# Kernel optimization log

Measured on AMD Instinct MI355X. Metric: run time of the kernel, lower is better.

The kernel has to match this reference:

```python
import jax, jax.numpy as jnp
import numpy as np

N = 10000   # nodes
E = 320000  # edges
B = 4       # batch
D = 128     # in_dim == out_dim
H = 4       # heads
DH = D // H # 32, per-head dim
OUT_L = D // H  # per-layer out_fc output dim (out_dim/num_heads)
NEG_SLOPE = 0.1


def setup_inputs() -> dict:
    key = jax.random.key(0)
    ks = jax.random.split(key, 20)
    inp = {
        "features": jax.random.normal(ks[0], (B, N, D), dtype=jnp.float32),
        "src": jax.random.randint(ks[1], (E,), 0, N),
        "dst": jax.random.randint(ks[2], (E,), 0, N),
        "edge_w": jax.random.uniform(ks[3], (E,), dtype=jnp.float32),
    }
    s = 0.05
    for l in range(2):
        k = 4 + 5 * l
        inp[f"fc_w{l}"] = jax.random.normal(ks[k], (D, D), dtype=jnp.float32) * s
        inp[f"al{l}"] = jax.random.normal(ks[k + 1], (H, DH), dtype=jnp.float32) * s
        inp[f"ar{l}"] = jax.random.normal(ks[k + 2], (H, DH), dtype=jnp.float32) * s
        inp[f"out_w{l}"] = jax.random.normal(ks[k + 3], (OUT_L, DH), dtype=jnp.float32) * s
        inp[f"out_b{l}"] = jnp.zeros((OUT_L,), dtype=jnp.float32)
    inp["mlp_w"] = jax.random.normal(ks[14], (D, 2 * D), dtype=jnp.float32) * s
    inp["mlp_b"] = jnp.zeros((D,), dtype=jnp.float32)
    return inp


def _gat_layer(x, src, dst, w, fc_w, al, ar, out_w, out_b):
    # x: [B,N,D]
    feat = jnp.einsum("bnd,ed->bne", x, fc_w).reshape(B, N, H, DH)  # fc, no bias
    el = jnp.einsum("bnhd,hd->bnh", feat, al)  # [B,N,H]
    er = jnp.einsum("bnhd,hd->bnh", feat, ar)
    # per-edge scores, edge-major: [E,B,H]
    e = jnp.moveaxis(el[:, src] + er[:, dst], 1, 0)
    e = jnp.where(e > 0, e, NEG_SLOPE * e)        # LeakyReLU(0.1)
    e = e * w[:, None, None]                      # edge weight applied pre-softmax
    # edge-softmax over incoming edges of each dst node
    m = jax.ops.segment_max(e, dst, num_segments=N)
    m = jnp.where(jnp.isfinite(m), m, 0.0)
    ex = jnp.exp(e - m[dst])
    den = jax.ops.segment_sum(ex, dst, num_segments=N)[dst]
    a = ex / jnp.where(den == 0, 1.0, den)        # [E,B,H]
    # u_mul_e + sum aggregation
    feat_n = jnp.moveaxis(feat, 0, 1)             # [N,B,H,DH]
    msg = feat_n[src] * a[..., None]              # [E,B,H,DH]
    agg = jax.ops.segment_sum(msg, dst, num_segments=N)  # [N,B,H,DH]
    out = jax.nn.relu(jnp.einsum("nbhd,od->nbho", agg, out_w) + out_b)
    # transpose(0,1) then concat heads along feature dim -> [B,N,H*OUT_L]
    return jnp.moveaxis(out, 0, 1).reshape(B, N, H * OUT_L)


def reference(features, src, dst, edge_w,
              fc_w0, al0, ar0, out_w0, out_b0,
              fc_w1, al1, ar1, out_w1, out_b1,
              mlp_w, mlp_b):
    x1 = _gat_layer(features, src, dst, edge_w, fc_w0, al0, ar0, out_w0, out_b0)
    x2 = _gat_layer(x1, src, dst, edge_w, fc_w1, al1, ar1, out_w1, out_b1)
    h = jnp.concatenate([x1, x2], axis=-1)        # [B,N,2*D]
    return jnp.einsum("bnk,ok->bno", h, mlp_w) + mlp_b  # eval mode: dropout off
```

## Files before the change

### kernel.cpp

```cpp
#include <hip/hip_runtime.h>
#include <hip/hip_fp16.h>
#include <float.h>

#define NN 10000
#define EE 320000
#define BB 4
#define DD 128
#define HH 4
#define DHH 32
#define CHUNK 128

union H4 { uint2 u2; __half2 h2[2]; };

typedef _Float16 f16x8 __attribute__((ext_vector_type(8)));
typedef float f32x4 __attribute__((ext_vector_type(4)));

__global__ void pack_weights(const float* __restrict__ fc0, const float* __restrict__ fc1,
                             const float* __restrict__ mlp,
                             __half* __restrict__ bp0, __half* __restrict__ bp1,
                             __half* __restrict__ bpm) {
    int s = blockIdx.x * 256 + threadIdx.x;
    int i = s & 7, l = (s >> 3) & 63, ct = (s >> 9) & 7, kt = s >> 12;
    int k = kt * 32 + 8 * (l >> 4) + i;
    int o = ct * 16 + (l & 15);
    bpm[s] = __float2half(mlp[o * 256 + k]);
    if (s < 16384) {
        bp0[s] = __float2half(fc0[o * 128 + k]);
        bp1[s] = __float2half(fc1[o * 128 + k]);
    }
}

__global__ void count_edges(const int* __restrict__ dst, int* __restrict__ cnt) {
    int e = blockIdx.x * 256 + threadIdx.x;
    if (e < EE) atomicAdd(&cnt[dst[e]], 1);
}

__global__ void scan_kernel(const int* __restrict__ cnt, int* __restrict__ row_off) {
    __shared__ int part[1024];
    int t = threadIdx.x;
    const int CH = 10;
    int loc[CH];
    int s = 0;
#pragma unroll
    for (int j = 0; j < CH; ++j) {
        int i = t * CH + j;
        int v = (i < NN) ? cnt[i] : 0;
        loc[j] = s;
        s += v;
    }
    part[t] = s;
    __syncthreads();
    for (int off = 1; off < 1024; off <<= 1) {
        int v = (t >= off) ? part[t - off] : 0;
        __syncthreads();
        part[t] += v;
        __syncthreads();
    }
    int pre = (t > 0) ? part[t - 1] : 0;
#pragma unroll
    for (int j = 0; j < CH; ++j) {
        int i = t * CH + j;
        if (i < NN) row_off[i] = pre + loc[j];
    }
    if (t == 0) row_off[NN] = part[1023];
}

__global__ void scatter_edges(const int* __restrict__ dst, const int* __restrict__ row_off,
                              int* __restrict__ cursor, int* __restrict__ edge_ids) {
    int e = blockIdx.x * 256 + threadIdx.x;
    if (e < EE) {
        int d = dst[e];
        int p = atomicAdd(&cursor[d], 1);
        edge_ids[row_off[d] + p] = e;
    }
}

template <int K, bool A_HALF, bool HALF_OUT, bool BIAS>
__global__ __launch_bounds__(256) void mfma_gemm(
    const void* __restrict__ A_, int lda,
    const __half* __restrict__ Bp,
    const float* __restrict__ bias,
    __half* __restrict__ outh, float* __restrict__ outf, int ldo) {
    __shared__ __half A_s[64 * K];
    int tid = threadIdx.x;
    int row0 = blockIdx.x * 64;

    if (A_HALF) {
        const __half* A = (const __half*)A_;
#pragma unroll
        for (int it = 0; it < (64 * K / 8) / 256; ++it) {
            int s = it * 256 + tid;
            int r = s / (K / 8), c8 = s % (K / 8);
            uint4 v = *reinterpret_cast<const uint4*>(A + (size_t)(row0 + r) * lda + c8 * 8);
            int byte = (r * K + c8 * 8) * 2;
            byte ^= (r & 7) << 4;
            *reinterpret_cast<uint4*>((char*)A_s + byte) = v;
        }
    } else {
        const float* A = (const float*)A_;
#pragma unroll
        for (int it = 0; it < (64 * K / 4) / 256; ++it) {
            int s = it * 256 + tid;
            int r = s / (K / 4), c4 = s % (K / 4);
            float4 v = *reinterpret_cast<const float4*>(A + (size_t)(row0 + r) * lda + c4 * 4);
            __half h[4];
            h[0] = __float2half(v.x); h[1] = __float2half(v.y);
            h[2] = __float2half(v.z); h[3] = __float2half(v.w);
            int byte = (r * K + c4 * 4) * 2;
            byte ^= (r & 7) << 4;
            *reinterpret_cast<uint2*>((char*)A_s + byte) = *reinterpret_cast<uint2*>(h);
        }
    }
    __syncthreads();

    int l = tid & 63, w = tid >> 6;
    int g = l >> 4, r15 = l & 15;
    f32x4 acc[8] = {};

#pragma unroll
    for (int kt = 0; kt < K / 32; ++kt) {
        int row = w * 16 + r15;
        int byte = (row * K + kt * 32 + 8 * g) * 2;
        byte ^= (row & 7) << 4;
        f16x8 a = *reinterpret_cast<const f16x8*>((const char*)A_s + byte);
        const f16x8* bp = reinterpret_cast<const f16x8*>(Bp) + (size_t)(kt * 8) * 64 + l;
#pragma unroll
        for (int ct = 0; ct < 8; ++ct) {
            f16x8 b = bp[(size_t)ct * 64];
            acc[ct] = __builtin_amdgcn_mfma_f32_16x16x32_f16(a, b, acc[ct], 0, 0, 0);
        }
    }

#pragma unroll
    for (int ct = 0; ct < 8; ++ct) {
        int col = ct * 16 + r15;
#pragma unroll
        for (int reg = 0; reg < 4; ++reg) {
            int row = row0 + w * 16 + g * 4 + reg;
            float v = acc[ct][reg];
            if (BIAS) v += bias[col];
            if (HALF_OUT) outh[(size_t)row * ldo + col] = __float2half(v);
            else outf[(size_t)row * ldo + col] = v;
        }
    }
}

__global__ __launch_bounds__(256) void elr_kernel(
    const __half* __restrict__ feat_h, const float* __restrict__ al,
    const float* __restrict__ ar, float* __restrict__ el, float* __restrict__ er) {
    __shared__ float s_al[128], s_ar[128];
    int tid = threadIdx.x;
    if (tid < 128) s_al[tid] = al[tid];
    else s_ar[tid - 128] = ar[tid - 128];
    __syncthreads();
    int idx = blockIdx.x * 256 + tid;
    if (idx < BB * NN * HH) {
        int h = idx & 3;
        const __half* row = feat_h + (size_t)(idx >> 2) * 128 + h * 32;
        float al_acc = 0.f, ar_acc = 0.f;
#pragma unroll
        for (int q = 0; q < 8; ++q) {
            H4 u;
            u.u2 = *reinterpret_cast<const uint2*>(row + q * 4);
            float2 f0 = __half22float2(u.h2[0]);
            float2 f1 = __half22float2(u.h2[1]);
            int d = h * 32 + q * 4;
            al_acc += f0.x * s_al[d] + f0.y * s_al[d + 1] + f1.x * s_al[d + 2] + f1.y * s_al[d + 3];
            ar_acc += f0.x * s_ar[d] + f0.y * s_ar[d + 1] + f1.x * s_ar[d + 2] + f1.y * s_ar[d + 3];
        }
        el[idx] = al_acc;
        er[idx] = ar_acc;
    }
}

__global__ __launch_bounds__(128) void gat_aggregate(
    const int* __restrict__ row_off, const int* __restrict__ edge_ids,
    const int* __restrict__ src, const float* __restrict__ ew,
    const float* __restrict__ el, const float* __restrict__ er,
    const __half* __restrict__ feat_h, const float* __restrict__ out_w,
    const float* __restrict__ out_b, __half* __restrict__ hcat, int layer_off) {
    __shared__ int s_src[CHUNK];
    __shared__ float s_w[CHUNK];
    __shared__ float s_red[8][16];
    __shared__ float s_m[16];
    __shared__ float s_scale[16];
    __shared__ float s_den[16];
    __shared__ float s_union[16 * 132];

    int tid = threadIdx.x;
    int n = blockIdx.x;
    int start = row_off[n], end = row_off[n + 1];

    int bh1 = tid & 15, js = tid >> 4;
    int b1 = bh1 >> 2, h1 = bh1 & 3;
    float er1 = er[((size_t)b1 * NN + n) * 4 + h1];

    int bh2 = tid >> 3, dq = tid & 7;
    int b2 = bh2 >> 2, h2 = bh2 & 3;
    const __half* fbase = feat_h + (size_t)b2 * NN * 128 + h2 * 32 + dq * 4;

    if (tid < 16) { s_m[tid] = -FLT_MAX; s_den[tid] = 0.f; }
    float4 acc = make_float4(0.f, 0.f, 0.f, 0.f);
    __syncthreads();

    for (int base = start; base < end; base += CHUNK) {
        int cnum = end - base;
        if (cnum > CHUNK) cnum = CHUNK;
        for (int j = tid; j < cnum; j += 128) {
            int eid = edge_ids[base + j];
            s_src[j] = src[eid];
            s_w[j] = ew[eid];
        }
        __syncthreads();
        float lmax = -FLT_MAX;
        for (int j = js; j < cnum; j += 8) {
            int s = s_src[j];
            float sc = el[((size_t)b1 * NN + s) * 4 + h1] + er1;
            sc = sc > 0.f ? sc : 0.1f * sc;
            sc *= s_w[j];
            s_union[bh1 * 132 + j] = sc;
            lmax = fmaxf(lmax, sc);
        }
        s_red[js][bh1] = lmax;
        __syncthreads();
        if (tid < 16) {
            float m_c = s_red[0][tid];
#pragma unroll
            for (int k = 1; k < 8; ++k) m_c = fmaxf(m_c, s_red[k][tid]);
            float m_old = s_m[tid];
            float m_new = fmaxf(m_old, m_c);
            s_scale[tid] = __expf(m_old - m_new);
            s_m[tid] = m_new;
        }
        __syncthreads();
        float lden = 0.f;
        float m_b = s_m[bh1];
        for (int j = js; j < cnum; j += 8) {
            float p = __expf(s_union[bh1 * 132 + j] - m_b);
            s_union[bh1 * 132 + j] = p;
            lden += p;
        }
        s_red[js][bh1] = lden;
        __syncthreads();
        if (tid < 16) {
            float d_c = 0.f;
#pragma unroll
            for (int k = 0; k < 8; ++k) d_c += s_red[k][tid];
            s_den[tid] = s_den[tid] * s_scale[tid] + d_c;
        }
        float sc2 = s_scale[bh2];
        acc.x *= sc2; acc.y *= sc2; acc.z *= sc2; acc.w *= sc2;
        const float* prow = s_union + bh2 * 132;
#pragma unroll 4
        for (int j = 0; j < cnum; ++j) {
            float p = prow[j];
            int s = s_src[j];
            H4 u;
            u.u2 = *reinterpret_cast<const uint2*>(fbase + (size_t)s * 128);
            float2 f0 = __half22float2(u.h2[0]);
            float2 f1 = __half22float2(u.h2[1]);
            acc.x += p * f0.x; acc.y += p * f0.y;
            acc.z += p * f1.x; acc.w += p * f1.y;
        }
        __syncthreads();
    }
    __syncthreads();

    for (int i = tid; i < 1024; i += 128) {
        int o = i >> 5, d = i & 31;
        s_union[d * 33 + o] = out_w[i];
    }
    float den_v = s_den[bh2];
    float inv_den = (den_v == 0.f) ? 1.f : 1.f / den_v;
    float* accl = s_union + 1056;
    accl[bh2 * 33 + dq * 4 + 0] = acc.x * inv_den;
    accl[bh2 * 33 + dq * 4 + 1] = acc.y * inv_den;
    accl[bh2 * 33 + dq * 4 + 2] = acc.z * inv_den;
    accl[bh2 * 33 + dq * 4 + 3] = acc.w * inv_den;
    __syncthreads();

    float o0 = out_b[dq * 4 + 0], o1 = out_b[dq * 4 + 1];
    float o2 = out_b[dq * 4 + 2], o3 = out_b[dq * 4 + 3];
    const float* accr = accl + bh2 * 33;
#pragma unroll 8
    for (int dd = 0; dd < 32; ++dd) {
        float a = accr[dd];
        const float* wr = s_union + dd * 33 + dq * 4;
        o0 += a * wr[0]; o1 += a * wr[1]; o2 += a * wr[2]; o3 += a * wr[3];
    }
    H4 ov;
    ov.h2[0] = __floats2half2_rn(fmaxf(o0, 0.f), fmaxf(o1, 0.f));
    ov.h2[1] = __floats2half2_rn(fmaxf(o2, 0.f), fmaxf(o3, 0.f));
    *reinterpret_cast<uint2*>(hcat + ((size_t)b2 * NN + n) * 256 + layer_off + h2 * 32 + dq * 4) = ov.u2;
}

extern "C" void kernel_launch(void* const* d_in, const int* in_sizes, int n_in,
                              void* d_out, int out_size, void* d_ws, size_t ws_size,
                              hipStream_t stream) {
    const float* features = (const float*)d_in[0];
    const int* src = (const int*)d_in[1];
    const int* dst = (const int*)d_in[2];
    const float* edge_w = (const float*)d_in[3];
    const float* fc_w0 = (const float*)d_in[4];
    const float* al0 = (const float*)d_in[5];
    const float* ar0 = (const float*)d_in[6];
    const float* out_w0 = (const float*)d_in[7];
    const float* out_b0 = (const float*)d_in[8];
    const float* fc_w1 = (const float*)d_in[9];
    const float* al1 = (const float*)d_in[10];
    const float* ar1 = (const float*)d_in[11];
    const float* out_w1 = (const float*)d_in[12];
    const float* out_b1 = (const float*)d_in[13];
    const float* mlp_w = (const float*)d_in[14];
    const float* mlp_b = (const float*)d_in[15];
    float* out = (float*)d_out;

    char* p = (char*)d_ws;
    auto take = [&](size_t bytes) {
        char* cur = p;
        p += (bytes + 255) & ~(size_t)255;
        return cur;
    };
    __half* bp0 = (__half*)take(16384 * 2);
    __half* bp1 = (__half*)take(16384 * 2);
    __half* bpm = (__half*)take(32768 * 2);
    __half* feat_h = (__half*)take((size_t)BB * NN * 128 * 2);
    __half* hcat = (__half*)take((size_t)BB * NN * 256 * 2);
    float* el = (float*)take((size_t)BB * NN * HH * 4);
    float* er = (float*)take((size_t)BB * NN * HH * 4);
    int* cnt = (int*)take((size_t)NN * 4);
    int* cursor = (int*)take((size_t)NN * 4);
    int* row_off = (int*)take((size_t)(NN + 1) * 4);
    int* edge_ids = (int*)take((size_t)EE * 4);
    (void)ws_size; (void)in_sizes; (void)n_in; (void)out_size;

    pack_weights<<<128, 256, 0, stream>>>(fc_w0, fc_w1, mlp_w, bp0, bp1, bpm);
    hipMemsetAsync(cnt, 0, (size_t)NN * 4, stream);
    hipMemsetAsync(cursor, 0, (size_t)NN * 4, stream);
    count_edges<<<EE / 256, 256, 0, stream>>>(dst, cnt);
    scan_kernel<<<1, 1024, 0, stream>>>(cnt, row_off);
    scatter_edges<<<EE / 256, 256, 0, stream>>>(dst, row_off, cursor, edge_ids);

    const int GEMM_GRID = (BB * NN) / 64;
    const int ELR_GRID = (BB * NN * HH + 255) / 256;

    mfma_gemm<128, false, true, false><<<GEMM_GRID, 256, 0, stream>>>(
        features, 128, bp0, nullptr, feat_h, nullptr, 128);
    elr_kernel<<<ELR_GRID, 256, 0, stream>>>(feat_h, al0, ar0, el, er);
    gat_aggregate<<<NN, 128, 0, stream>>>(row_off, edge_ids, src, edge_w, el, er,
                                          feat_h, out_w0, out_b0, hcat, 0);
    mfma_gemm<128, true, true, false><<<GEMM_GRID, 256, 0, stream>>>(
        hcat, 256, bp1, nullptr, feat_h, nullptr, 128);
    elr_kernel<<<ELR_GRID, 256, 0, stream>>>(feat_h, al1, ar1, el, er);
    gat_aggregate<<<NN, 128, 0, stream>>>(row_off, edge_ids, src, edge_w, el, er,
                                          feat_h, out_w1, out_b1, hcat, 128);
    mfma_gemm<256, true, false, true><<<GEMM_GRID, 256, 0, stream>>>(
        hcat, 256, bpm, mlp_b, nullptr, out, 128);
}
```

Before: 213.1 us.

## Map one wavefront per destination node in GAT aggregation, drop block barriers

The aggregation kernel now handles four destination nodes per 256-thread block, with one 64-lane wavefront per node. The online-softmax max and denominator reductions use cross-lane shuffles instead of shared-memory reductions and __syncthreads. Each lane gathers 8 halves (16 bytes) per edge instead of 4. The two hipMemsetAsync calls are folded into the pack_weights kernel to save launches. This removes many block-wide barriers and idle threads for low-degree nodes. The risk is that intra-wave shared-memory reuse now relies on implicit wavefront lockstep and higher register use per lane.

```diff
diff --git a/kernel.cpp b/kernel.cpp
--- a/kernel.cpp
+++ b/kernel.cpp
@@ -8,9 +8,9 @@
 #define DD 128
 #define HH 4
 #define DHH 32
-#define CHUNK 128
 
 union H4 { uint2 u2; __half2 h2[2]; };
+union H8 { float4 f4; __half2 h2[4]; };
 
 typedef _Float16 f16x8 __attribute__((ext_vector_type(8)));
 typedef float f32x4 __attribute__((ext_vector_type(4)));
@@ -18,7 +18,8 @@
 __global__ void pack_weights(const float* __restrict__ fc0, const float* __restrict__ fc1,
                              const float* __restrict__ mlp,
                              __half* __restrict__ bp0, __half* __restrict__ bp1,
-                             __half* __restrict__ bpm) {
+                             __half* __restrict__ bpm,
+                             int* __restrict__ cnt, int* __restrict__ cursor) {
     int s = blockIdx.x * 256 + threadIdx.x;
     int i = s & 7, l = (s >> 3) & 63, ct = (s >> 9) & 7, kt = s >> 12;
     int k = kt * 32 + 8 * (l >> 4) + i;
@@ -28,6 +29,7 @@
         bp0[s] = __float2half(fc0[o * 128 + k]);
         bp1[s] = __float2half(fc1[o * 128 + k]);
     }
+    if (s < NN) { cnt[s] = 0; cursor[s] = 0; }
 }
 
 __global__ void count_edges(const int* __restrict__ dst, int* __restrict__ cnt) {
@@ -173,125 +175,113 @@
     }
 }
 
-__global__ __launch_bounds__(128) void gat_aggregate(
+#define PSTR 66
+__global__ __launch_bounds__(256) void gat_aggregate(
     const int* __restrict__ row_off, const int* __restrict__ edge_ids,
     const int* __restrict__ src, const float* __restrict__ ew,
     const float* __restrict__ el, const float* __restrict__ er,
     const __half* __restrict__ feat_h, const float* __restrict__ out_w,
     const float* __restrict__ out_b, __half* __restrict__ hcat, int layer_off) {
-    __shared__ int s_src[CHUNK];
-    __shared__ float s_w[CHUNK];
-    __shared__ float s_red[8][16];
-    __shared__ float s_m[16];
-    __shared__ float s_scale[16];
-    __shared__ float s_den[16];
-    __shared__ float s_union[16 * 132];
+    __shared__ float s_owt[32 * 33];
+    __shared__ int s_srcA[4][64];
+    __shared__ float s_wA[4][64];
+    __shared__ float s_pA[4][16 * PSTR];
 
     int tid = threadIdx.x;
-    int n = blockIdx.x;
+    for (int i = tid; i < 1024; i += 256) {
+        int o = i >> 5, d = i & 31;
+        s_owt[d * 33 + o] = out_w[i];
+    }
+    __syncthreads();
+
+    int wv = tid >> 6, lane = tid & 63;
+    int n = blockIdx.x * 4 + wv;
     int start = row_off[n], end = row_off[n + 1];
-
-    int bh1 = tid & 15, js = tid >> 4;
-    int b1 = bh1 >> 2, h1 = bh1 & 3;
-    float er1 = er[((size_t)b1 * NN + n) * 4 + h1];
-
-    int bh2 = tid >> 3, dq = tid & 7;
-    int b2 = bh2 >> 2, h2 = bh2 & 3;
-    const __half* fbase = feat_h + (size_t)b2 * NN * 128 + h2 * 32 + dq * 4;
-
-    if (tid < 16) { s_m[tid] = -FLT_MAX; s_den[tid] = 0.f; }
-    float4 acc = make_float4(0.f, 0.f, 0.f, 0.f);
-    __syncthreads();
-
-    for (int base = start; base < end; base += CHUNK) {
+    int* s_src = s_srcA[wv];
+    float* s_w = s_wA[wv];
+    float* s_p = s_pA[wv];
+
+    int bh = lane & 15, sl = lane >> 4;
+    int b = bh >> 2, h = bh & 3;
+    float er1 = er[((size_t)b * NN + n) * 4 + h];
+    const __half* fbase = feat_h + (size_t)b * NN * 128 + h * 32 + sl * 8;
+
+    float m_reg = -FLT_MAX, den_reg = 0.f;
+    float acc8[8];
+#pragma unroll
+    for (int i = 0; i < 8; ++i) acc8[i] = 0.f;
+
+    for (int base = start; base < end; base += 64) {
         int cnum = end - base;
-        if (cnum > CHUNK) cnum = CHUNK;
-        for (int j = tid; j < cnum; j += 128) {
-            int eid = edge_ids[base + j];
-            s_src[j] = src[eid];
-            s_w[j] = ew[eid];
-        }
-        __syncthreads();
+        if (cnum > 64) cnum = 64;
+        if (lane < cnum) {
+            int eid = edge_ids[base + lane];
+            s_src[lane] = src[eid];
+            s_w[lane] = ew[eid];
+        }
         float lmax = -FLT_MAX;
-        for (int j = js; j < cnum; j += 8) {
+#pragma unroll 4
+        for (int j = sl; j < cnum; j += 4) {
             int s = s_src[j];
-            float sc = el[((size_t)b1 * NN + s) * 4 + h1] + er1;
+            float sc = el[((size_t)b * NN + s) * 4 + h] + er1;
             sc = sc > 0.f ? sc : 0.1f * sc;
             sc *= s_w[j];
-            s_union[bh1 * 132 + j] = sc;
+            s_p[bh * PSTR + j] = sc;
             lmax = fmaxf(lmax, sc);
         }
-        s_red[js][bh1] = lmax;
-        __syncthreads();
-        if (tid < 16) {
-            float m_c = s_red[0][tid];
-#pragma unroll
-            for (int k = 1; k < 8; ++k) m_c = fmaxf(m_c, s_red[k][tid]);
-            float m_old = s_m[tid];
-            float m_new = fmaxf(m_old, m_c);
-            s_scale[tid] = __expf(m_old - m_new);
-            s_m[tid] = m_new;
-        }
-        __syncthreads();
+        lmax = fmaxf(lmax, __shfl_xor(lmax, 16, 64));
+        lmax = fmaxf(lmax, __shfl_xor(lmax, 32, 64));
+        float m_new = fmaxf(m_reg, lmax);
+        float scale = __expf(m_reg - m_new);
+        m_reg = m_new;
         float lden = 0.f;
-        float m_b = s_m[bh1];
-        for (int j = js; j < cnum; j += 8) {
-            float p = __expf(s_union[bh1 * 132 + j] - m_b);
-            s_union[bh1 * 132 + j] = p;
+#pragma unroll 4
+        for (int j = sl; j < cnum; j += 4) {
+            float p = __expf(s_p[bh * PSTR + j] - m_new);
+            s_p[bh * PSTR + j] = p;
             lden += p;
         }
-        s_red[js][bh1] = lden;
-        __syncthreads();
-        if (tid < 16) {
-            float d_c = 0.f;
-#pragma unroll
-            for (int k = 0; k < 8; ++k) d_c += s_red[k][tid];
-            s_den[tid] = s_den[tid] * s_scale[tid] + d_c;
-        }
-        float sc2 = s_scale[bh2];
-        acc.x *= sc2; acc.y *= sc2; acc.z *= sc2; acc.w *= sc2;
-        const float* prow = s_union + bh2 * 132;
-#pragma unroll 4
+        lden += __shfl_xor(lden, 16, 64);
+        lden += __shfl_xor(lden, 32, 64);
+        den_reg = den_reg * scale + lden;
+#pragma unroll
+        for (int i = 0; i < 8; ++i) acc8[i] *= scale;
+#pragma unroll 8
         for (int j = 0; j < cnum; ++j) {
-            float p = prow[j];
+            float p = s_p[bh * PSTR + j];
             int s = s_src[j];
-            H4 u;
-            u.u2 = *reinterpret_cast<const uint2*>(fbase + (size_t)s * 128);
+            H8 u;
+            u.f4 = *reinterpret_cast<const float4*>(fbase + (size_t)s * 128);
             float2 f0 = __half22float2(u.h2[0]);
             float2 f1 = __half22float2(u.h2[1]);
-            acc.x += p * f0.x; acc.y += p * f0.y;
-            acc.z += p * f1.x; acc.w += p * f1.y;
-        }
-        __syncthreads();
-    }
-    __syncthreads();
-
-    for (int i = tid; i < 1024; i += 128) {
-        int o = i >> 5, d = i & 31;
-        s_union[d * 33 + o] = out_w[i];
-    }
-    float den_v = s_den[bh2];
-    float inv_den = (den_v == 0.f) ? 1.f : 1.f / den_v;
-    float* accl = s_union + 1056;
-    accl[bh2 * 33 + dq * 4 + 0] = acc.x * inv_den;
-    accl[bh2 * 33 + dq * 4 + 1] = acc.y * inv_den;
-    accl[bh2 * 33 + dq * 4 + 2] = acc.z * inv_den;
-    accl[bh2 * 33 + dq * 4 + 3] = acc.w * inv_den;
-    __syncthreads();
-
-    float o0 = out_b[dq * 4 + 0], o1 = out_b[dq * 4 + 1];
-    float o2 = out_b[dq * 4 + 2], o3 = out_b[dq * 4 + 3];
-    const float* accr = accl + bh2 * 33;
+            float2 f2 = __half22float2(u.h2[2]);
+            float2 f3 = __half22float2(u.h2[3]);
+            acc8[0] += p * f0.x; acc8[1] += p * f0.y;
+            acc8[2] += p * f1.x; acc8[3] += p * f1.y;
+            acc8[4] += p * f2.x; acc8[5] += p * f2.y;
+            acc8[6] += p * f3.x; acc8[7] += p * f3.y;
+        }
+    }
+
+    float inv_den = (den_reg == 0.f) ? 1.f : 1.f / den_reg;
+#pragma unroll
+    for (int i = 0; i < 8; ++i) s_p[bh * PSTR + sl * 8 + i] = acc8[i] * inv_den;
+
+    float o_acc[8];
+#pragma unroll
+    for (int i = 0; i < 8; ++i) o_acc[i] = out_b[sl * 8 + i];
 #pragma unroll 8
     for (int dd = 0; dd < 32; ++dd) {
-        float a = accr[dd];
-        const float* wr = s_union + dd * 33 + dq * 4;
-        o0 += a * wr[0]; o1 += a * wr[1]; o2 += a * wr[2]; o3 += a * wr[3];
-    }
-    H4 ov;
-    ov.h2[0] = __floats2half2_rn(fmaxf(o0, 0.f), fmaxf(o1, 0.f));
-    ov.h2[1] = __floats2half2_rn(fmaxf(o2, 0.f), fmaxf(o3, 0.f));
-    *reinterpret_cast<uint2*>(hcat + ((size_t)b2 * NN + n) * 256 + layer_off + h2 * 32 + dq * 4) = ov.u2;
+        float a = s_p[bh * PSTR + dd];
+        const float* wr = s_owt + dd * 33 + sl * 8;
+#pragma unroll
+        for (int i = 0; i < 8; ++i) o_acc[i] += a * wr[i];
+    }
+    H8 ov;
+#pragma unroll
+    for (int k = 0; k < 4; ++k)
+        ov.h2[k] = __floats2half2_rn(fmaxf(o_acc[2 * k], 0.f), fmaxf(o_acc[2 * k + 1], 0.f));
+    *reinterpret_cast<float4*>(hcat + ((size_t)b * NN + n) * 256 + layer_off + h * 32 + sl * 8) = ov.f4;
 }
 
 extern "C" void kernel_launch(void* const* d_in, const int* in_sizes, int n_in,
@@ -334,26 +324,25 @@
     int* edge_ids = (int*)take((size_t)EE * 4);
     (void)ws_size; (void)in_sizes; (void)n_in; (void)out_size;
 
-    pack_weights<<<128, 256, 0, stream>>>(fc_w0, fc_w1, mlp_w, bp0, bp1, bpm);
-    hipMemsetAsync(cnt, 0, (size_t)NN * 4, stream);
-    hipMemsetAsync(cursor, 0, (size_t)NN * 4, stream);
+    pack_weights<<<128, 256, 0, stream>>>(fc_w0, fc_w1, mlp_w, bp0, bp1, bpm, cnt, cursor);
     count_edges<<<EE / 256, 256, 0, stream>>>(dst, cnt);
     scan_kernel<<<1, 1024, 0, stream>>>(cnt, row_off);
     scatter_edges<<<EE / 256, 256, 0, stream>>>(dst, row_off, cursor, edge_ids);
 
     const int GEMM_GRID = (BB * NN) / 64;
     const int ELR_GRID = (BB * NN * HH + 255) / 256;
+    const int AGG_GRID = NN / 4;
 
     mfma_gemm<128, false, true, false><<<GEMM_GRID, 256, 0, stream>>>(
         features, 128, bp0, nullptr, feat_h, nullptr, 128);
     elr_kernel<<<ELR_GRID, 256, 0, stream>>>(feat_h, al0, ar0, el, er);
-    gat_aggregate<<<NN, 128, 0, stream>>>(row_off, edge_ids, src, edge_w, el, er,
-                                          feat_h, out_w0, out_b0, hcat, 0);
+    gat_aggregate<<<AGG_GRID, 256, 0, stream>>>(row_off, edge_ids, src, edge_w, el, er,
+                                                feat_h, out_w0, out_b0, hcat, 0);
     mfma_gemm<128, true, true, false><<<GEMM_GRID, 256, 0, stream>>>(
         hcat, 256, bp1, nullptr, feat_h, nullptr, 128);
     elr_kernel<<<ELR_GRID, 256, 0, stream>>>(feat_h, al1, ar1, el, er);
-    gat_aggregate<<<NN, 128, 0, stream>>>(row_off, edge_ids, src, edge_w, el, er,
-                                          feat_h, out_w1, out_b1, hcat, 128);
+    gat_aggregate<<<AGG_GRID, 256, 0, stream>>>(row_off, edge_ids, src, edge_w, el, er,
+                                                feat_h, out_w1, out_b1, hcat, 128);
     mfma_gemm<256, true, false, true><<<GEMM_GRID, 256, 0, stream>>>(
         hcat, 256, bpm, mlp_b, nullptr, out, 128);
 }
```

After: 211.2 us. No clear change (-0.9%).
